# Kernel tuning notes

Measured on AMD Instinct MI355X. Metric: run time of the kernel, lower is better.

## Reference

```python
import jax, jax.numpy as jnp
import numpy as np

D_IN = 1024
D_OUT = 1024
NUM_HEADS = 16
HEAD_DIM = D_OUT // NUM_HEADS
SEQ = 2048
BATCH = 4


def setup_inputs() -> dict:
    key = jax.random.key(0)
    ks = jax.random.split(key, 6)
    s_in = 1.0 / np.sqrt(D_IN)
    s_out = 1.0 / np.sqrt(D_OUT)
    return {
        "inputs": jax.random.normal(ks[0], (BATCH, SEQ, D_IN), dtype=jnp.float32),
        # nn.Linear stores weight as [out, in]; y = x @ W.T
        "W_q": jax.random.uniform(ks[1], (D_OUT, D_IN), jnp.float32, -s_in, s_in),
        "W_k": jax.random.uniform(ks[2], (D_OUT, D_IN), jnp.float32, -s_in, s_in),
        "W_v": jax.random.uniform(ks[3], (D_OUT, D_IN), jnp.float32, -s_in, s_in),
        "W_o": jax.random.uniform(ks[4], (D_OUT, D_OUT), jnp.float32, -s_out, s_out),
        "b_o": jax.random.uniform(ks[5], (D_OUT,), jnp.float32, -s_out, s_out),
    }


def reference(inputs, W_q, W_k, W_v, W_o, b_o):
    B, T, _ = inputs.shape
    # projections: [B, T, d_out] -> [B, H, T, hd]
    def split_heads(x):
        return x.reshape(B, T, NUM_HEADS, HEAD_DIM).transpose(0, 2, 1, 3)

    Q = split_heads(inputs @ W_q.T)
    K = split_heads(inputs @ W_k.T)
    V = split_heads(inputs @ W_v.T)

    # [B, H, T, T] causal attention scores
    scores = jnp.einsum("bhqd,bhkd->bhqk", Q, K)
    causal = jnp.tril(jnp.ones((T, T), dtype=bool))  # True = keep
    scores = jnp.where(causal, scores, -jnp.inf)
    weights = jax.nn.softmax(scores / np.sqrt(HEAD_DIM), axis=-1)
    # dropout p=0.0 (eval mode): identity

    ctx = jnp.einsum("bhqk,bhkd->bhqd", weights, V)
    ctx = ctx.transpose(0, 2, 1, 3).reshape(B, T, D_OUT)
    return ctx @ W_o.T + b_o
```

## Files before the change

### kernel.cpp

```cpp
#include <hip/hip_runtime.h>
#include <cstdint>
#include <cstddef>

#define D_MODEL 1024
#define SEQQ    2048
#define NBATCH  4
#define NHEAD   16
#define HDIM    64
#define MTOT    (NBATCH * SEQQ)

typedef __attribute__((ext_vector_type(8))) short short8;
typedef __attribute__((ext_vector_type(4))) float floatx4;
typedef unsigned short u16;

__device__ __forceinline__ u16 f2bf(float f) {
  union { float f; uint32_t u; } a; a.f = f;
  uint32_t u = a.u;
  u += 0x7fffu + ((u >> 16) & 1u);
  return (u16)(u >> 16);
}

__device__ __forceinline__ floatx4 mfma16(short8 a, short8 b, floatx4 c) {
  return __builtin_amdgcn_mfma_f32_16x16x32_bf16(a, b, c, 0, 0, 0);
}

__device__ __forceinline__ void load_lds16(const void* g, void* l) {
  __builtin_amdgcn_global_load_lds(
      (const __attribute__((address_space(1))) uint32_t*)g,
      (__attribute__((address_space(3))) uint32_t*)l, 16, 0, 0);
}

__global__ __launch_bounds__(256) void k_cast_all(
    const float* __restrict__ X, const float* __restrict__ w0,
    const float* __restrict__ w1, const float* __restrict__ w2,
    const float* __restrict__ w3,
    u16* __restrict__ xb, u16* __restrict__ y0, u16* __restrict__ y1,
    u16* __restrict__ y2, u16* __restrict__ y3) {
  const int bx = blockIdx.x;
  const float* src; u16* dst; int i;
  if (bx < 8192) {
    src = X; dst = xb; i = (bx * 256 + threadIdx.x) * 4;
  } else {
    const int w = (bx - 8192) >> 10;
    src = (w == 0) ? w0 : (w == 1) ? w1 : (w == 2) ? w2 : w3;
    dst = (w == 0) ? y0 : (w == 1) ? y1 : (w == 2) ? y2 : y3;
    i = (((bx - 8192) & 1023) * 256 + threadIdx.x) * 4;
  }
  float4 v = *(const float4*)(src + i);
  ushort4 o;
  o.x = f2bf(v.x); o.y = f2bf(v.y); o.z = f2bf(v.z); o.w = f2bf(v.w);
  *(ushort4*)(dst + i) = o;
}

__global__ __launch_bounds__(256) void k_gemm_bt(
    const u16* __restrict__ A,
    const u16* __restrict__ B0, const u16* __restrict__ B1, const u16* __restrict__ B2,
    void* __restrict__ C0, void* __restrict__ C1, u16* __restrict__ VtOut,
    const float* __restrict__ bias, int M, int N, int K, int f32out, float ascaleQ) {
  __shared__ __align__(16) u16 As[2][128 * 64];
  __shared__ __align__(16) u16 Bs[2][128 * 64];
  const int tid = threadIdx.x;
  const int lane = tid & 63, wave = tid >> 6;
  const int quad = lane >> 4, l15 = lane & 15;

  const int bx = blockIdx.x;
  const int swz = (bx & 7) * 64 + (bx >> 3);
  const int m0 = (swz >> 3) * 128, n0 = (swz & 7) * 128;

  const int wr = wave >> 1, wc = wave & 1;
  const u16* Bm = (blockIdx.z == 0) ? B0 : (blockIdx.z == 1 ? B1 : B2);
  void* Cm = (blockIdx.z == 0) ? C0 : C1;
  const float ascale = (blockIdx.z == 0) ? ascaleQ : 1.0f;

  floatx4 acc[4][4];
#pragma unroll
  for (int i = 0; i < 4; ++i)
#pragma unroll
    for (int jj = 0; jj < 4; ++jj) acc[i][jj] = (floatx4){0.f, 0.f, 0.f, 0.f};

  const int srow = tid >> 3;
  const int scolx = ((tid & 7) * 8) ^ ((srow & 7) * 8);
  const u16* Ag = A + (size_t)(m0 + srow) * K + scolx;
  const u16* Bg = Bm + (size_t)(n0 + srow) * K + scolx;

#define STAGE_AB(tt, buf)                                                            \
  {                                                                                  \
    const int kk_ = (tt) * 64;                                                       \
    _Pragma("unroll")                                                                \
    for (int p = 0; p < 4; ++p) {                                                    \
      load_lds16(Ag + (size_t)(p * 32) * K + kk_, &As[buf][p * 2048 + wave * 512]);  \
      load_lds16(Bg + (size_t)(p * 32) * K + kk_, &Bs[buf][p * 2048 + wave * 512]);  \
    }                                                                                \
  }

  const int nIt = K / 64;
  STAGE_AB(0, 0);

  for (int it = 0; it < nIt; ++it) {
    const int cur = it & 1;
    __syncthreads();
    if (it + 1 < nIt) STAGE_AB(it + 1, cur ^ 1);

    short8 af[2][4], bfg[2][4];
#pragma unroll
    for (int ks = 0; ks < 2; ++ks) {
      const int kkx = (ks * 32 + quad * 8) ^ ((l15 & 7) * 8);
#pragma unroll
      for (int i = 0; i < 4; ++i) {
        af[ks][i]  = *(const short8*)&As[cur][(wr * 64 + i * 16 + l15) * 64 + kkx];
        bfg[ks][i] = *(const short8*)&Bs[cur][(wc * 64 + i * 16 + l15) * 64 + kkx];
      }
    }
#pragma unroll
    for (int ks = 0; ks < 2; ++ks)
#pragma unroll
      for (int mi = 0; mi < 4; ++mi)
#pragma unroll
        for (int ni = 0; ni < 4; ++ni)
          acc[mi][ni] = mfma16(af[ks][mi], bfg[ks][ni], acc[mi][ni]);
  }
#undef STAGE_AB

  if (blockIdx.z == 2) {
#pragma unroll
    for (int mi = 0; mi < 4; ++mi) {
#pragma unroll
      for (int ni = 0; ni < 4; ++ni) {
        const int row = m0 + wr * 64 + mi * 16 + quad * 4;
        const int col = n0 + wc * 64 + ni * 16 + l15;
        const int b = row >> 11, t = row & 2047;
        const int h = col >> 6, d = col & 63;
        ushort4 pk;
        pk.x = f2bf(acc[mi][ni][0]); pk.y = f2bf(acc[mi][ni][1]);
        pk.z = f2bf(acc[mi][ni][2]); pk.w = f2bf(acc[mi][ni][3]);
        *(ushort4*)(VtOut + (((size_t)(b * 16 + h) * 64 + d) * SEQQ + t)) = pk;
      }
    }
    return;
  }
#pragma unroll
  for (int mi = 0; mi < 4; ++mi) {
#pragma unroll
    for (int ni = 0; ni < 4; ++ni) {
      const int row = m0 + wr * 64 + mi * 16 + quad * 4;
      const int col = n0 + wc * 64 + ni * 16 + l15;
      const float bv = bias ? bias[col] : 0.f;
#pragma unroll
      for (int r = 0; r < 4; ++r) {
        const float v = acc[mi][ni][r] * ascale + bv;
        if (f32out) ((float*)Cm)[(size_t)(row + r) * N + col] = v;
        else        ((u16*)Cm)[(size_t)(row + r) * N + col] = f2bf(v);
      }
    }
  }
}

__device__ __forceinline__ short8 mk8(uint32_t a, uint32_t b, uint32_t c, uint32_t d) {
  union { uint32_t u[4]; short8 s; } t;
  t.u[0] = a; t.u[1] = b; t.u[2] = c; t.u[3] = d;
  return t.s;
}

__device__ __forceinline__ void softmax_reg(
    const floatx4 (&st)[4], float& lp, uint32_t (&w)[4][2]) {
#pragma unroll
  for (int ni = 0; ni < 4; ++ni) {
    const float p0 = __builtin_amdgcn_exp2f(st[ni][0]);
    const float p1 = __builtin_amdgcn_exp2f(st[ni][1]);
    const float p2 = __builtin_amdgcn_exp2f(st[ni][2]);
    const float p3 = __builtin_amdgcn_exp2f(st[ni][3]);
    lp += (p0 + p1) + (p2 + p3);
    w[ni][0] = __builtin_amdgcn_perm(__float_as_uint(p1), __float_as_uint(p0), 0x07060302u);
    w[ni][1] = __builtin_amdgcn_perm(__float_as_uint(p3), __float_as_uint(p2), 0x07060302u);
  }
}

__device__ __forceinline__ short8 pf_prep(const uint32_t (&w)[4][2], int kc) {
  uint32_t y0 = w[2 * kc][0], z0 = w[2 * kc + 1][0];
  asm("v_permlane32_swap_b32 %0, %1" : "+v"(y0), "+v"(z0));
  asm("v_permlane16_swap_b32 %0, %1" : "+v"(y0), "+v"(z0));
  uint32_t y1 = w[2 * kc][1], z1 = w[2 * kc + 1][1];
  asm("v_permlane32_swap_b32 %0, %1" : "+v"(y1), "+v"(z1));
  asm("v_permlane16_swap_b32 %0, %1" : "+v"(y1), "+v"(z1));
  return mk8(y0, y1, z0, z1);
}

__global__ __launch_bounds__(256, 2) void k_attn(
    const u16* __restrict__ Q, const u16* __restrict__ Kg,
    const u16* __restrict__ Vt, u16* __restrict__ O) {
  __shared__ __align__(16) u16 Ks[2][128 * 64];
  __shared__ __align__(16) u16 Vs[2][64 * 128];
  const int tid = threadIdx.x, lane = tid & 63, wave = tid >> 6;
  const int quad = lane >> 4, l15 = lane & 15;

  const int lin = blockIdx.x;
  const int c = lin & 255, k2 = lin >> 8;
  const int j = k2 ? (7 - (c & 7)) : (c & 7);
  const int bh = (c >> 3) | (k2 << 5);
  const int b = bh >> 4, h = bh & 15;

  const int s = wave;
  const int p1 = j, p2 = j + 8;
  int lim[4], qw[4];
  lim[0] = p1;      qw[0] = 64 * p1 + 16 * s;
  lim[1] = 31 - p1; qw[1] = SEQQ - 64 * (p1 + 1) + 16 * s;
  lim[2] = p2;      qw[2] = 64 * p2 + 16 * s;
  lim[3] = 31 - p2; qw[3] = SEQQ - 64 * (p2 + 1) + 16 * s;
  const int nSub = 32 - j;
  const int nT = (nSub + 1) >> 1;

  const u16* kbase = Kg + (size_t)(b * SEQQ) * D_MODEL + h * HDIM;
  const u16* vbase = Vt + (size_t)bh * (HDIM * SEQQ);

  const int krow = tid >> 3;
  const int kcol = ((tid & 7) * 8) ^ ((krow & 7) * 8);
  const int vrow = tid >> 4, vslot = tid & 15;
  const int vcol = (vslot >> 3) * 64 + (((vslot & 7) ^ (vrow & 7)) * 8);

#define STAGE_KV(tt, buf)                                                           \
  {                                                                                 \
    const int kt_ = (tt) * 128;                                                     \
    _Pragma("unroll")                                                               \
    for (int c4 = 0; c4 < 4; ++c4)                                                  \
      load_lds16(kbase + (size_t)(kt_ + c4 * 32 + krow) * D_MODEL + kcol,           \
                 &Ks[buf][c4 * 2048 + wave * 512]);                                 \
    _Pragma("unroll")                                                               \
    for (int c4 = 0; c4 < 4; ++c4)                                                  \
      load_lds16(vbase + (size_t)(c4 * 16 + vrow) * SEQQ + kt_ + vcol,              \
                 &Vs[buf][c4 * 2048 + wave * 512]);                                 \
  }

  STAGE_KV(0, 0);

  short8 qf[4][2];
#pragma unroll
  for (int t4 = 0; t4 < 4; ++t4) {
    const u16* qp = Q + (size_t)(b * SEQQ + qw[t4] + l15) * D_MODEL + h * HDIM;
#pragma unroll
    for (int ks = 0; ks < 2; ++ks)
      qf[t4][ks] = *(const short8*)(qp + ks * 32 + quad * 8);
  }

  floatx4 acc[4][4];
  float lp[4] = {0.f, 0.f, 0.f, 0.f};
#pragma unroll
  for (int t4 = 0; t4 < 4; ++t4)
#pragma unroll
    for (int i = 0; i < 4; ++i) acc[t4][i] = (floatx4){0.f, 0.f, 0.f, 0.f};

  for (int t = 0; t < nT; ++t) {
    const int cur = t & 1;
    __syncthreads();
    if (t + 1 < nT) STAGE_KV(t + 1, cur ^ 1);

#pragma unroll
    for (int sub = 0; sub < 2; ++sub) {
      const int u = 2 * t + sub;

      short8 kf[4][2];
#pragma unroll
      for (int ni = 0; ni < 4; ++ni)
#pragma unroll
        for (int ks = 0; ks < 2; ++ks)
          kf[ni][ks] = *(const short8*)&Ks[cur][(sub * 64 + ni * 16 + l15) * 64 +
                                               ((ks * 32 + quad * 8) ^ ((l15 & 7) * 8))];

      uint32_t w[4][4][2];
      bool act[4];
#pragma unroll
      for (int t4 = 0; t4 < 4; ++t4) {
        act[t4] = (u <= lim[t4]);
        if (act[t4]) {
          floatx4 st[4];
          __builtin_amdgcn_s_setprio(1);
#pragma unroll
          for (int ni = 0; ni < 4; ++ni) {
            floatx4 sv = (floatx4){0.f, 0.f, 0.f, 0.f};
            sv = mfma16(kf[ni][0], qf[t4][0], sv);
            sv = mfma16(kf[ni][1], qf[t4][1], sv);
            st[ni] = sv;
          }
          __builtin_amdgcn_s_setprio(0);
          if (u == lim[t4]) {
            const int qg = qw[t4] + l15;
#pragma unroll
            for (int ni = 0; ni < 4; ++ni) {
              const int kg = u * 64 + ni * 16 + quad * 4;
#pragma unroll
              for (int r = 0; r < 4; ++r)
                if (kg + r > qg) st[ni][r] = -1e30f;
            }
          }
          softmax_reg(st, lp[t4], w[t4]);
        }
      }

      short8 vf[2][4];
#pragma unroll
      for (int kc = 0; kc < 2; ++kc)
#pragma unroll
        for (int di = 0; di < 4; ++di)
          vf[kc][di] = *(const short8*)&Vs[cur][(di * 16 + l15) * 128 + sub * 64 +
                                               ((kc * 32 + quad * 8) ^ ((l15 & 7) * 8))];

#pragma unroll
      for (int kc = 0; kc < 2; ++kc) {
#pragma unroll
        for (int t4 = 0; t4 < 4; ++t4) {
          if (act[t4]) {
            const short8 pf = pf_prep(w[t4], kc);
            __builtin_amdgcn_s_setprio(1);
#pragma unroll
            for (int di = 0; di < 4; ++di)
              acc[t4][di] = mfma16(pf, vf[kc][di], acc[t4][di]);
            __builtin_amdgcn_s_setprio(0);
          }
        }
      }
    }
  }

#pragma unroll
  for (int t4 = 0; t4 < 4; ++t4) {
    float l = lp[t4];
    l += __shfl_xor(l, 16); l += __shfl_xor(l, 32);
    u16* orow = O + (size_t)(b * SEQQ + qw[t4] + quad * 4) * D_MODEL + h * HDIM + l15;
#pragma unroll
    for (int r = 0; r < 4; ++r) {
      const float inv = 1.0f / __shfl(l, quad * 4 + r, 16);
#pragma unroll
      for (int di = 0; di < 4; ++di)
        orow[(size_t)r * D_MODEL + di * 16] = f2bf(acc[t4][di][r] * inv);
    }
  }
}

extern "C" void kernel_launch(void* const* d_in, const int* in_sizes, int n_in,
                              void* d_out, int out_size, void* d_ws, size_t ws_size,
                              hipStream_t stream) {
  const float* X  = (const float*)d_in[0];
  const float* Wq = (const float*)d_in[1];
  const float* Wk = (const float*)d_in[2];
  const float* Wv = (const float*)d_in[3];
  const float* Wo = (const float*)d_in[4];
  const float* bo = (const float*)d_in[5];
  float* out = (float*)d_out;

  u16* ws = (u16*)d_ws;
  const size_t NE = (size_t)MTOT * D_MODEL;
  u16* Xb  = ws;
  u16* Qb  = Xb + NE;
  u16* Kb  = Qb + NE;
  u16* Vt  = Kb + NE;
  u16* Cb  = Vt + NE;
  u16* Wqb = Cb + NE;
  u16* Wkb = Wqb + (size_t)D_MODEL * D_MODEL;
  u16* Wvb = Wkb + (size_t)D_MODEL * D_MODEL;
  u16* Wob = Wvb + (size_t)D_MODEL * D_MODEL;

  const float SCL2E = 0.18033688f;

  k_cast_all<<<12288, 256, 0, stream>>>(X, Wq, Wk, Wv, Wo, Xb, Wqb, Wkb, Wvb, Wob);

  k_gemm_bt<<<dim3(512, 1, 3), 256, 0, stream>>>(
      Xb, Wqb, Wkb, Wvb, Qb, Kb, Vt, nullptr, MTOT, D_MODEL, D_MODEL, 0, SCL2E);

  k_attn<<<512, 256, 0, stream>>>(Qb, Kb, Vt, Cb);

  k_gemm_bt<<<dim3(512, 1, 1), 256, 0, stream>>>(
      Cb, Wob, Wob, Wob, out, out, nullptr, bo, MTOT, D_MODEL, D_MODEL, 1, 1.0f);
}
```

Baseline: 243.8 us.

## Fuse QKV into one GEMM with 256x128 tiles and triple-buffered LDS

The GEMM kernel moves from 128x128 tiles with 4 waves and double buffering to 256x128 tiles with 8 waves and a 3-stage LDS pipeline. It uses explicit vmcnt waits and raw barriers so two tiles of loads are in flight while the current one is computed. The three Q/K/V projections become a single N=3072 GEMM that reads the contiguous Wq/Wk/Wv workspace, and the epilogue routes each column to the Q, K or transposed-V output. The intent is to raise arithmetic intensity, hide global-load latency and drop the blockIdx.z-based splitting. In exchange it uses about 147KB of LDS, which limits each CU to one block, and it relies on the three weight buffers being adjacent in memory.

```diff
diff --git a/kernel.cpp b/kernel.cpp
--- a/kernel.cpp
+++ b/kernel.cpp
@@ -52,25 +52,22 @@
   *(ushort4*)(dst + i) = o;
 }
 
-__global__ __launch_bounds__(256) void k_gemm_bt(
-    const u16* __restrict__ A,
-    const u16* __restrict__ B0, const u16* __restrict__ B1, const u16* __restrict__ B2,
-    void* __restrict__ C0, void* __restrict__ C1, u16* __restrict__ VtOut,
-    const float* __restrict__ bias, int M, int N, int K, int f32out, float ascaleQ) {
-  __shared__ __align__(16) u16 As[2][128 * 64];
-  __shared__ __align__(16) u16 Bs[2][128 * 64];
+__global__ __launch_bounds__(512) void k_gemm_bt(
+    const u16* __restrict__ A, const u16* __restrict__ B,
+    u16* __restrict__ Oq, u16* __restrict__ Ok, u16* __restrict__ OVt,
+    float* __restrict__ Of32, const float* __restrict__ bias,
+    int K, int NT, int mode, float ascaleQ) {
+  __shared__ __align__(16) u16 As[3][256 * 64];
+  __shared__ __align__(16) u16 Bs[3][128 * 64];
   const int tid = threadIdx.x;
   const int lane = tid & 63, wave = tid >> 6;
   const int quad = lane >> 4, l15 = lane & 15;
+  const int wr = wave >> 1, wc = wave & 1;
 
   const int bx = blockIdx.x;
-  const int swz = (bx & 7) * 64 + (bx >> 3);
-  const int m0 = (swz >> 3) * 128, n0 = (swz & 7) * 128;
-
-  const int wr = wave >> 1, wc = wave & 1;
-  const u16* Bm = (blockIdx.z == 0) ? B0 : (blockIdx.z == 1 ? B1 : B2);
-  void* Cm = (blockIdx.z == 0) ? C0 : C1;
-  const float ascale = (blockIdx.z == 0) ? ascaleQ : 1.0f;
+  const int cpx = (NT * 32) >> 3;
+  const int swz = (bx & 7) * cpx + (bx >> 3);
+  const int m0 = (swz / NT) * 256, n0 = (swz % NT) * 128;
 
   floatx4 acc[4][4];
 #pragma unroll
@@ -81,75 +78,97 @@
   const int srow = tid >> 3;
   const int scolx = ((tid & 7) * 8) ^ ((srow & 7) * 8);
   const u16* Ag = A + (size_t)(m0 + srow) * K + scolx;
-  const u16* Bg = Bm + (size_t)(n0 + srow) * K + scolx;
-
-#define STAGE_AB(tt, buf)                                                            \
-  {                                                                                  \
-    const int kk_ = (tt) * 64;                                                       \
-    _Pragma("unroll")                                                                \
-    for (int p = 0; p < 4; ++p) {                                                    \
-      load_lds16(Ag + (size_t)(p * 32) * K + kk_, &As[buf][p * 2048 + wave * 512]);  \
-      load_lds16(Bg + (size_t)(p * 32) * K + kk_, &Bs[buf][p * 2048 + wave * 512]);  \
-    }                                                                                \
+  const u16* Bg = B + (size_t)(n0 + srow) * K + scolx;
+
+#define STAGE(tt, buf)                                                              \
+  {                                                                                 \
+    const int kk_ = (tt) * 64;                                                      \
+    _Pragma("unroll")                                                               \
+    for (int c4 = 0; c4 < 4; ++c4)                                                  \
+      load_lds16(Ag + (size_t)(c4 * 64) * K + kk_,                                  \
+                 &As[buf][c4 * 4096 + wave * 512]);                                 \
+    _Pragma("unroll")                                                               \
+    for (int c4 = 0; c4 < 2; ++c4)                                                  \
+      load_lds16(Bg + (size_t)(c4 * 64) * K + kk_,                                  \
+                 &Bs[buf][c4 * 4096 + wave * 512]);                                 \
+  }
+
+#define COMPUTE(curb)                                                               \
+  {                                                                                 \
+    short8 af[2][4], bfg[2][4];                                                     \
+    _Pragma("unroll")                                                               \
+    for (int ks = 0; ks < 2; ++ks) {                                                \
+      const int kkx = (ks * 32 + quad * 8) ^ ((l15 & 7) * 8);                       \
+      _Pragma("unroll")                                                             \
+      for (int i = 0; i < 4; ++i) {                                                 \
+        af[ks][i]  = *(const short8*)&As[curb][(wr * 64 + i * 16 + l15) * 64 + kkx];\
+        bfg[ks][i] = *(const short8*)&Bs[curb][(wc * 64 + i * 16 + l15) * 64 + kkx];\
+      }                                                                             \
+    }                                                                               \
+    _Pragma("unroll")                                                               \
+    for (int ks = 0; ks < 2; ++ks)                                                  \
+      _Pragma("unroll")                                                             \
+      for (int mi = 0; mi < 4; ++mi)                                                \
+        _Pragma("unroll")                                                           \
+        for (int ni = 0; ni < 4; ++ni)                                              \
+          acc[mi][ni] = mfma16(af[ks][mi], bfg[ks][ni], acc[mi][ni]);               \
   }
 
   const int nIt = K / 64;
-  STAGE_AB(0, 0);
-
-  for (int it = 0; it < nIt; ++it) {
-    const int cur = it & 1;
-    __syncthreads();
-    if (it + 1 < nIt) STAGE_AB(it + 1, cur ^ 1);
-
-    short8 af[2][4], bfg[2][4];
-#pragma unroll
-    for (int ks = 0; ks < 2; ++ks) {
-      const int kkx = (ks * 32 + quad * 8) ^ ((l15 & 7) * 8);
-#pragma unroll
-      for (int i = 0; i < 4; ++i) {
-        af[ks][i]  = *(const short8*)&As[cur][(wr * 64 + i * 16 + l15) * 64 + kkx];
-        bfg[ks][i] = *(const short8*)&Bs[cur][(wc * 64 + i * 16 + l15) * 64 + kkx];
-      }
-    }
-#pragma unroll
-    for (int ks = 0; ks < 2; ++ks)
-#pragma unroll
-      for (int mi = 0; mi < 4; ++mi)
-#pragma unroll
-        for (int ni = 0; ni < 4; ++ni)
-          acc[mi][ni] = mfma16(af[ks][mi], bfg[ks][ni], acc[mi][ni]);
-  }
-#undef STAGE_AB
-
-  if (blockIdx.z == 2) {
+  STAGE(0, 0);
+  STAGE(1, 1);
+  asm volatile("s_waitcnt vmcnt(6)" ::: "memory");
+  asm volatile("s_barrier" ::: "memory");
+
+  for (int it = 0; it + 2 < nIt; ++it) {
+    const int cur = it % 3;
+    STAGE(it + 2, (it + 2) % 3);
+    COMPUTE(cur);
+    asm volatile("s_waitcnt vmcnt(6)" ::: "memory");
+    asm volatile("s_barrier" ::: "memory");
+  }
+  COMPUTE((nIt - 2) % 3);
+  asm volatile("s_waitcnt vmcnt(0)" ::: "memory");
+  asm volatile("s_barrier" ::: "memory");
+  COMPUTE((nIt - 1) % 3);
+#undef STAGE
+#undef COMPUTE
+
+  if (mode == 0) {
 #pragma unroll
     for (int mi = 0; mi < 4; ++mi) {
 #pragma unroll
       for (int ni = 0; ni < 4; ++ni) {
         const int row = m0 + wr * 64 + mi * 16 + quad * 4;
         const int col = n0 + wc * 64 + ni * 16 + l15;
-        const int b = row >> 11, t = row & 2047;
-        const int h = col >> 6, d = col & 63;
-        ushort4 pk;
-        pk.x = f2bf(acc[mi][ni][0]); pk.y = f2bf(acc[mi][ni][1]);
-        pk.z = f2bf(acc[mi][ni][2]); pk.w = f2bf(acc[mi][ni][3]);
-        *(ushort4*)(VtOut + (((size_t)(b * 16 + h) * 64 + d) * SEQQ + t)) = pk;
+        const int proj = col >> 10, cw = col & 1023;
+        if (proj == 2) {
+          const int b = row >> 11, t = row & 2047;
+          const int h = cw >> 6, d = cw & 63;
+          ushort4 pk;
+          pk.x = f2bf(acc[mi][ni][0]); pk.y = f2bf(acc[mi][ni][1]);
+          pk.z = f2bf(acc[mi][ni][2]); pk.w = f2bf(acc[mi][ni][3]);
+          *(ushort4*)(OVt + (((size_t)(b * 16 + h) * 64 + d) * SEQQ + t)) = pk;
+        } else {
+          const float sc = (proj == 0) ? ascaleQ : 1.0f;
+          u16* dst = (proj == 0) ? Oq : Ok;
+#pragma unroll
+          for (int r = 0; r < 4; ++r)
+            dst[(size_t)(row + r) * 1024 + cw] = f2bf(acc[mi][ni][r] * sc);
+        }
       }
     }
-    return;
-  }
-#pragma unroll
-  for (int mi = 0; mi < 4; ++mi) {
-#pragma unroll
-    for (int ni = 0; ni < 4; ++ni) {
-      const int row = m0 + wr * 64 + mi * 16 + quad * 4;
-      const int col = n0 + wc * 64 + ni * 16 + l15;
-      const float bv = bias ? bias[col] : 0.f;
-#pragma unroll
-      for (int r = 0; r < 4; ++r) {
-        const float v = acc[mi][ni][r] * ascale + bv;
-        if (f32out) ((float*)Cm)[(size_t)(row + r) * N + col] = v;
-        else        ((u16*)Cm)[(size_t)(row + r) * N + col] = f2bf(v);
+  } else {
+#pragma unroll
+    for (int mi = 0; mi < 4; ++mi) {
+#pragma unroll
+      for (int ni = 0; ni < 4; ++ni) {
+        const int row = m0 + wr * 64 + mi * 16 + quad * 4;
+        const int col = n0 + wc * 64 + ni * 16 + l15;
+        const float bv = bias[col];
+#pragma unroll
+        for (int r = 0; r < 4; ++r)
+          Of32[(size_t)(row + r) * 1024 + col] = acc[mi][ni][r] + bv;
       }
     }
   }
@@ -362,11 +381,11 @@
 
   k_cast_all<<<12288, 256, 0, stream>>>(X, Wq, Wk, Wv, Wo, Xb, Wqb, Wkb, Wvb, Wob);
 
-  k_gemm_bt<<<dim3(512, 1, 3), 256, 0, stream>>>(
-      Xb, Wqb, Wkb, Wvb, Qb, Kb, Vt, nullptr, MTOT, D_MODEL, D_MODEL, 0, SCL2E);
+  k_gemm_bt<<<768, 512, 0, stream>>>(
+      Xb, Wqb, Qb, Kb, Vt, nullptr, nullptr, D_MODEL, 24, 0, SCL2E);
 
   k_attn<<<512, 256, 0, stream>>>(Qb, Kb, Vt, Cb);
 
-  k_gemm_bt<<<dim3(512, 1, 1), 256, 0, stream>>>(
-      Cb, Wob, Wob, Wob, out, out, nullptr, bo, MTOT, D_MODEL, D_MODEL, 1, 1.0f);
-}
+  k_gemm_bt<<<256, 512, 0, stream>>>(
+      Cb, Wob, nullptr, nullptr, nullptr, out, bo, D_MODEL, 8, 1, 1.0f);
+}
```

Measured after the change: 267.6 us. 1.1x slower.

## Load GEMM B operand directly from global into registers, bypassing LDS

Applied to the files above, without the earlier changes.

The projection GEMM no longer stages the B (weight) tile through shared memory. Each wave loads its B fragments straight from global memory into registers, double-buffered across two register sets, while A stays double-buffered in LDS. The loop is unrolled by two to alternate buffers. This halves LDS traffic and footprint, which may raise occupancy, but it adds register pressure and relies on uncoalesced 16-byte global loads that are duplicated across the waves sharing a column.

```diff
diff --git a/kernel.cpp b/kernel.cpp
--- a/kernel.cpp
+++ b/kernel.cpp
@@ -58,7 +58,6 @@
     void* __restrict__ C0, void* __restrict__ C1, u16* __restrict__ VtOut,
     const float* __restrict__ bias, int M, int N, int K, int f32out, float ascaleQ) {
   __shared__ __align__(16) u16 As[2][128 * 64];
-  __shared__ __align__(16) u16 Bs[2][128 * 64];
   const int tid = threadIdx.x;
   const int lane = tid & 63, wave = tid >> 6;
   const int quad = lane >> 4, l15 = lane & 15;
@@ -81,45 +80,58 @@
   const int srow = tid >> 3;
   const int scolx = ((tid & 7) * 8) ^ ((srow & 7) * 8);
   const u16* Ag = A + (size_t)(m0 + srow) * K + scolx;
-  const u16* Bg = Bm + (size_t)(n0 + srow) * K + scolx;
-
-#define STAGE_AB(tt, buf)                                                            \
+  const u16* Bf = Bm + (size_t)(n0 + wc * 64 + l15) * K + quad * 8;
+
+#define STAGE_A(tt, buf)                                                             \
   {                                                                                  \
     const int kk_ = (tt) * 64;                                                       \
     _Pragma("unroll")                                                                \
-    for (int p = 0; p < 4; ++p) {                                                    \
+    for (int p = 0; p < 4; ++p)                                                      \
       load_lds16(Ag + (size_t)(p * 32) * K + kk_, &As[buf][p * 2048 + wave * 512]);  \
-      load_lds16(Bg + (size_t)(p * 32) * K + kk_, &Bs[buf][p * 2048 + wave * 512]);  \
+  }
+
+#define PREFETCH_B(tt, SET)                                                          \
+  _Pragma("unroll")                                                                  \
+  for (int ks = 0; ks < 2; ++ks)                                                     \
+    _Pragma("unroll")                                                                \
+    for (int i = 0; i < 4; ++i)                                                      \
+      SET[ks][i] = *(const short8*)(Bf + (size_t)(i * 16) * K + (tt) * 64 + ks * 32);
+
+#define COMPUTE(curb, SET)                                                           \
+  {                                                                                  \
+    short8 af[2][4];                                                                 \
+    _Pragma("unroll")                                                                \
+    for (int ks = 0; ks < 2; ++ks) {                                                 \
+      const int kkx = (ks * 32 + quad * 8) ^ ((l15 & 7) * 8);                        \
+      _Pragma("unroll")                                                              \
+      for (int i = 0; i < 4; ++i)                                                    \
+        af[ks][i] = *(const short8*)&As[curb][(wr * 64 + i * 16 + l15) * 64 + kkx];  \
     }                                                                                \
+    _Pragma("unroll")                                                                \
+    for (int ks = 0; ks < 2; ++ks)                                                   \
+      _Pragma("unroll")                                                              \
+      for (int mi = 0; mi < 4; ++mi)                                                 \
+        _Pragma("unroll")                                                            \
+        for (int ni = 0; ni < 4; ++ni)                                               \
+          acc[mi][ni] = mfma16(af[ks][mi], SET[ks][ni], acc[mi][ni]);                \
   }
 
   const int nIt = K / 64;
-  STAGE_AB(0, 0);
-
-  for (int it = 0; it < nIt; ++it) {
-    const int cur = it & 1;
+  short8 bA[2][4], bB[2][4];
+  STAGE_A(0, 0);
+  PREFETCH_B(0, bA);
+
+  for (int it = 0; it < nIt; it += 2) {
     __syncthreads();
-    if (it + 1 < nIt) STAGE_AB(it + 1, cur ^ 1);
-
-    short8 af[2][4], bfg[2][4];
-#pragma unroll
-    for (int ks = 0; ks < 2; ++ks) {
-      const int kkx = (ks * 32 + quad * 8) ^ ((l15 & 7) * 8);
-#pragma unroll
-      for (int i = 0; i < 4; ++i) {
-        af[ks][i]  = *(const short8*)&As[cur][(wr * 64 + i * 16 + l15) * 64 + kkx];
-        bfg[ks][i] = *(const short8*)&Bs[cur][(wc * 64 + i * 16 + l15) * 64 + kkx];
-      }
-    }
-#pragma unroll
-    for (int ks = 0; ks < 2; ++ks)
-#pragma unroll
-      for (int mi = 0; mi < 4; ++mi)
-#pragma unroll
-        for (int ni = 0; ni < 4; ++ni)
-          acc[mi][ni] = mfma16(af[ks][mi], bfg[ks][ni], acc[mi][ni]);
-  }
-#undef STAGE_AB
+    if (it + 1 < nIt) { STAGE_A(it + 1, 1); PREFETCH_B(it + 1, bB); }
+    COMPUTE(0, bA);
+    __syncthreads();
+    if (it + 2 < nIt) { STAGE_A(it + 2, 0); PREFETCH_B(it + 2, bA); }
+    COMPUTE(1, bB);
+  }
+#undef STAGE_A
+#undef PREFETCH_B
+#undef COMPUTE
 
   if (blockIdx.z == 2) {
 #pragma unroll
```

After: 306.9 us. 1.26x slower.
